# Kernel tuning notes

Hardware: AMD Instinct MI355X
Metric: run time of the kernel (lower is better)

The kernel has to match this reference:

```python
import jax, jax.numpy as jnp
import numpy as np

EPS = 1e-12  # matches torch F.normalize default eps

def l2norm(t):
    n = jnp.linalg.norm(t, axis=-1, keepdims=True)
    return t / jnp.maximum(n, EPS)

def rotate_half(x):
    # '... (j d) -> ... j d' with j=2: split into two halves, return cat(-x2, x1)
    x1, x2 = jnp.split(x, 2, axis=-1)
    return jnp.concatenate((-x2, x1), axis=-1)

def rotary_freqs(seq_len, dim):
    inv_freq = 1.0 / (10000.0 ** (jnp.arange(0, dim, 2, dtype=jnp.float32) / dim))
    seq = jnp.arange(seq_len, dtype=jnp.float32)
    freqs = seq[:, None] * inv_freq[None, :]          # [n, d/2]
    emb = jnp.concatenate((freqs, freqs), axis=-1)    # [n, d]
    return emb[None, None]                            # [1, 1, n, d]

def apply_rotary_pos_emb(t, freqs):
    # rot_dim == dim_head here, so the pass-through slice is empty
    return t * jnp.cos(freqs) + rotate_half(t) * jnp.sin(freqs)

def setup_inputs() -> dict:
    key = jax.random.key(0)
    kq, kk, kv = jax.random.split(key, 3)
    b, h, n, d = 2, 16, 2048, 64
    q = jax.random.normal(kq, (b, h, n, d), dtype=jnp.float32)
    k = jax.random.normal(kk, (b, h, n, d), dtype=jnp.float32)
    v = jax.random.normal(kv, (b, h, n, d), dtype=jnp.float32)
    q_scale = jnp.ones((d,), dtype=jnp.float32)
    k_scale = jnp.ones((d,), dtype=jnp.float32)
    return {"q": q, "k": k, "v": v, "q_scale": q_scale, "k_scale": k_scale}

def reference(q, k, v, q_scale, k_scale):
    b, h, n, d = q.shape
    # QK RMSNorm (l2 normalize + learned per-dim scale)
    q = l2norm(q) * q_scale
    k = l2norm(k) * k_scale
    # rotary position embedding (always applied in the source module)
    freqs = rotary_freqs(n, d)
    q = apply_rotary_pos_emb(q, freqs)
    k = apply_rotary_pos_emb(k, freqs)
    # attention: explicit scores -> softmax -> values
    scale = d ** -0.5
    sim = jnp.einsum('bhid,bhjd->bhij', q, k) * scale
    attn = jax.nn.softmax(sim, axis=-1)
    out = jnp.einsum('bhij,bhjd->bhid', attn, v)
    # 'b h n d -> b n (h d)'
    return out.transpose(0, 2, 1, 3).reshape(b, n, h * d)
```

## Files before the change

kernel.cpp:

```cpp
#include <hip/hip_runtime.h>
#include <math.h>

#define BH   32
#define NSEQ 2048
#define DH   64
#define NH   16
#define LOG2E 1.44269504088896f

typedef _Float16 f16x8 __attribute__((ext_vector_type(8)));
typedef __fp16   fp16x2 __attribute__((ext_vector_type(2)));
typedef _Float16 half2v __attribute__((ext_vector_type(2)));
typedef float    f32x16v __attribute__((ext_vector_type(16)));
typedef unsigned uint2v __attribute__((ext_vector_type(2)));

#if __has_builtin(__builtin_amdgcn_exp2f)
#define EXP2F(x) __builtin_amdgcn_exp2f(x)
#else
#define EXP2F(x) exp2f(x)
#endif

static __device__ __forceinline__ unsigned pkrtz(float a, float b) {
    fp16x2 r = __builtin_amdgcn_cvt_pkrtz(a, b);
    return __builtin_bit_cast(unsigned, r);
}
static __device__ __forceinline__ unsigned packh_rne(float a, float b) {
    union { _Float16 h[2]; unsigned u; } x;
    x.h[0] = (_Float16)a; x.h[1] = (_Float16)b;
    return x.u;
}

static __device__ __forceinline__ float2 rope_cs(int pos, int p) {
    float invf_rev = EXP2F(-(float)p * (13.287712379549449f / 32.0f)) * 0.15915494309189535f;
    float rev = (float)pos * invf_rev;
    float fr = rev - floorf(rev);
    float th = fr * 6.283185307179586f;
    return make_float2(__cosf(th), __sinf(th));
}

__global__ __launch_bounds__(256) void rope_tab_kernel(float4* __restrict__ tab) {
    const int id = blockIdx.x * 256 + threadIdx.x;
    const int pos = id >> 4, j = id & 15;
    float2 a = rope_cs(pos, 2 * j);
    float2 b = rope_cs(pos, 2 * j + 1);
    tab[id] = make_float4(a.x, a.y, b.x, b.y);
}

__global__ __launch_bounds__(256) void prep_all(
    const float* __restrict__ q, const float* __restrict__ k, const float* __restrict__ v,
    const float* __restrict__ qs, const float* __restrict__ ksc,
    const float4* __restrict__ tab,
    unsigned* __restrict__ qh, unsigned* __restrict__ kh, unsigned* __restrict__ vt2) {
    const int bid = blockIdx.x;
    const int t = threadIdx.x;
    if (bid < 4096) {
        const bool isq = bid < 2048;
        const float* in = isq ? q : k;
        const float* sc = isq ? qs : ksc;
        const float smul = isq ? 0.125f * LOG2E : 1.0f;
        const int sb = bid & 2047;
        const int r = t >> 3, l = t & 7;
        const int row = sb * 32 + r;
        const int pos = row & (NSEQ - 1);
        const float4* tb = tab + (pos << 4) + 4 * l;
        const float4 c0 = tb[0], c1 = tb[1], c2 = tb[2], c3 = tb[3];
        const float4 xa = *(const float4*)(in + (size_t)row * DH + 8 * l);
        const float4 xb = *(const float4*)(in + (size_t)row * DH + 8 * l + 4);
        float ss = xa.x * xa.x + xa.y * xa.y + xa.z * xa.z + xa.w * xa.w
                 + xb.x * xb.x + xb.y * xb.y + xb.z * xb.z + xb.w * xb.w;
        ss += __shfl_xor(ss, 1);
        ss += __shfl_xor(ss, 2);
        ss += __shfl_xor(ss, 4);
        const float inv = 1.0f / fmaxf(sqrtf(ss), 1e-12f);
        const float4 sa = *(const float4*)(sc + 8 * l);
        const float4 sb4 = *(const float4*)(sc + 8 * l + 4);
        float tv[8];
        tv[0] = xa.x * inv * sa.x;  tv[1] = xa.y * inv * sa.y;
        tv[2] = xa.z * inv * sa.z;  tv[3] = xa.w * inv * sa.w;
        tv[4] = xb.x * inv * sb4.x; tv[5] = xb.y * inv * sb4.y;
        tv[6] = xb.z * inv * sb4.z; tv[7] = xb.w * inv * sb4.w;
        float rv[8];
        #pragma unroll
        for (int e = 0; e < 8; ++e) {
            float p = __shfl_xor(tv[e], 4);
            rv[e] = (l < 4) ? -p : p;
        }
        float ov[8];
        ov[0] = (tv[0] * c0.x + rv[0] * c0.y) * smul;
        ov[1] = (tv[1] * c0.z + rv[1] * c0.w) * smul;
        ov[2] = (tv[2] * c1.x + rv[2] * c1.y) * smul;
        ov[3] = (tv[3] * c1.z + rv[3] * c1.w) * smul;
        ov[4] = (tv[4] * c2.x + rv[4] * c2.y) * smul;
        ov[5] = (tv[5] * c2.z + rv[5] * c2.w) * smul;
        ov[6] = (tv[6] * c3.x + rv[6] * c3.y) * smul;
        ov[7] = (tv[7] * c3.z + rv[7] * c3.w) * smul;
        const uint4 u4 = make_uint4(packh_rne(ov[0], ov[1]), packh_rne(ov[2], ov[3]),
                                    packh_rne(ov[4], ov[5]), packh_rne(ov[6], ov[7]));
        if (isq) {
            *(uint4*)(qh + row * 32 + 4 * l) = u4;
        } else {
            const int rloc = row & (NSEQ - 1);
            const unsigned idx = (unsigned)((rloc >> 5) * 1024 + (l >> 1) * 256
                               + (l & 1) * 128 + (rloc & 31) * 4);
            *(uint4*)(kh + (size_t)(row >> 11) * 65536 + idx) = u4;
        }
    } else {
        const int sb = bid - 4096;
        const int kt = sb & 31, bh = sb >> 5;
        __shared__ float Lv[64 * 68];
        #pragma unroll
        for (int i = 0; i < 4; ++i) {
            int chunk = t + 256 * i;
            int rr = chunk >> 4, fg = chunk & 15;
            *(float4*)&Lv[rr * 68 + fg * 4] =
                *(const float4*)(v + ((size_t)bh * NSEQ + kt * 64 + rr) * DH + fg * 4);
        }
        __syncthreads();
        const int d = t & 63, kg = t >> 6;
        unsigned u[8];
        #pragma unroll
        for (int j = 0; j < 8; ++j) {
            int ky = kg * 16 + 2 * j;
            u[j] = pkrtz(Lv[ky * 68 + d], Lv[(ky + 1) * 68 + d]);
        }
        const int rh = d >> 5, cc = d & 31;
        unsigned* dst = vt2 + (size_t)bh * 65536
                      + (size_t)((kt * 4 + kg) * 2 + rh) * 256 + cc * 4;
        *(uint4*)(dst)       = make_uint4(u[0], u[1], u[2], u[3]);
        *(uint4*)(dst + 128) = make_uint4(u[4], u[5], u[6], u[7]);
    }
}

static __device__ __forceinline__ f16x8 ld8(const unsigned* p) {
    return *(const f16x8*)p;
}

static __device__ __forceinline__ void load_k(f16x8 (&kd)[4], const unsigned* p) {
    #pragma unroll
    for (int ks = 0; ks < 4; ++ks) kd[ks] = ld8(p + ks * 256);
}
static __device__ __forceinline__ void load_v(f16x8 (&vd)[4], const unsigned* p) {
    #pragma unroll
    for (int kk = 0; kk < 2; ++kk)
        #pragma unroll
        for (int rh = 0; rh < 2; ++rh)
            vd[kk * 2 + rh] = ld8(p + kk * 512 + rh * 256);
}

static __device__ __forceinline__ void qk2(
    const f16x8 (&kc)[4], const f16x8 (&qf)[2][4], const f32x16v& z16,
    f32x16v& s0, f32x16v& s1)
{
    __builtin_amdgcn_s_setprio(1);
    s0 = __builtin_amdgcn_mfma_f32_32x32x16_f16(kc[0], qf[0][0], z16, 0, 0, 0);
    s1 = __builtin_amdgcn_mfma_f32_32x32x16_f16(kc[0], qf[1][0], z16, 0, 0, 0);
    #pragma unroll
    for (int ks = 1; ks < 4; ++ks) {
        s0 = __builtin_amdgcn_mfma_f32_32x32x16_f16(kc[ks], qf[0][ks], s0, 0, 0, 0);
        s1 = __builtin_amdgcn_mfma_f32_32x32x16_f16(kc[ks], qf[1][ks], s1, 0, 0, 0);
    }
    __builtin_amdgcn_s_setprio(0);
}

static __device__ __forceinline__ void pv_tile(
    f32x16v& s, const f16x8 (&vc)[4], f32x16v (&ot)[2], float& lp, int hf)
{
    #pragma unroll
    for (int r = 0; r < 16; ++r) s[r] = EXP2F(s[r]);
    #pragma unroll
    for (int kk = 0; kk < 2; ++kk) {
        unsigned P01 = pkrtz(s[kk * 8 + 0], s[kk * 8 + 1]);
        unsigned P23 = pkrtz(s[kk * 8 + 2], s[kk * 8 + 3]);
        unsigned P45 = pkrtz(s[kk * 8 + 4], s[kk * 8 + 5]);
        unsigned P67 = pkrtz(s[kk * 8 + 6], s[kk * 8 + 7]);
#if __has_builtin(__builtin_amdgcn_fdot2)
        const half2v one2 = {(_Float16)1.0f, (_Float16)1.0f};
        lp = __builtin_amdgcn_fdot2(__builtin_bit_cast(half2v, P01), one2, lp, false);
        lp = __builtin_amdgcn_fdot2(__builtin_bit_cast(half2v, P23), one2, lp, false);
        lp = __builtin_amdgcn_fdot2(__builtin_bit_cast(half2v, P45), one2, lp, false);
        lp = __builtin_amdgcn_fdot2(__builtin_bit_cast(half2v, P67), one2, lp, false);
#else
        #pragma unroll
        for (int r = 0; r < 8; ++r) lp += s[kk * 8 + r];
#endif
        union { unsigned u[4]; f16x8 v; } B;
#if __has_builtin(__builtin_amdgcn_permlane32_swap)
        uint2v r02 = __builtin_amdgcn_permlane32_swap(P01, P45, 0, 0);
        uint2v r13 = __builtin_amdgcn_permlane32_swap(P23, P67, 0, 0);
        B.u[0] = r02[0]; B.u[1] = r13[0]; B.u[2] = r02[1]; B.u[3] = r13[1];
#else
        unsigned x01 = (unsigned)__shfl_xor((int)P01, 32);
        unsigned x23 = (unsigned)__shfl_xor((int)P23, 32);
        unsigned x45 = (unsigned)__shfl_xor((int)P45, 32);
        unsigned x67 = (unsigned)__shfl_xor((int)P67, 32);
        B.u[0] = hf ? x45 : P01;
        B.u[1] = hf ? x67 : P23;
        B.u[2] = hf ? P45 : x01;
        B.u[3] = hf ? P67 : x23;
#endif
        __builtin_amdgcn_s_setprio(1);
        ot[0] = __builtin_amdgcn_mfma_f32_32x32x16_f16(vc[kk * 2 + 0], B.v, ot[0], 0, 0, 0);
        ot[1] = __builtin_amdgcn_mfma_f32_32x32x16_f16(vc[kk * 2 + 1], B.v, ot[1], 0, 0, 0);
        __builtin_amdgcn_s_setprio(0);
    }
}

static __device__ __forceinline__ void smpv2(
    f32x16v& s0, f32x16v& s1, const f16x8 (&vc)[4],
    f32x16v (&o)[2][2], float (&lp)[2], int hf)
{
    pv_tile(s0, vc, o[0], lp[0], hf);
    pv_tile(s1, vc, o[1], lp[1], hf);
}

__global__ __launch_bounds__(256, 2) void attn_kernel(
    const unsigned* __restrict__ qh, const unsigned* __restrict__ kf,
    const unsigned* __restrict__ vf, float* __restrict__ out) {

    __shared__ float Lred[128 * 33];

    const int flat = (blockIdx.x & 7) * 64 + (blockIdx.x >> 3);
    const int bh = flat >> 4, qb = flat & 15;

    const int tid = threadIdx.x;
    const int w = tid >> 6, lane = tid & 63;
    const int c = lane & 31, hf = lane >> 5;
    const int qhw = w & 1;
    const int khw = w >> 1;

    const _Float16* qbase = (const _Float16*)qh + ((size_t)bh * NSEQ + qb * 128) * DH;
    f16x8 qf[2][4];
    #pragma unroll
    for (int t = 0; t < 2; ++t)
        #pragma unroll
        for (int ks = 0; ks < 4; ++ks)
            qf[t][ks] = *(const f16x8*)(qbase + (t * 64 + qhw * 32 + c) * DH + ks * 16 + hf * 8);

    const unsigned* kfb = kf + (size_t)bh * 65536 + khw * 1024 + lane * 4;
    const unsigned* vfb = vf + (size_t)bh * 65536 + khw * 1024 + lane * 4;

    f32x16v z16;
    #pragma unroll
    for (int r = 0; r < 16; ++r) z16[r] = 0.f;

    f32x16v o[2][2];
    #pragma unroll
    for (int t = 0; t < 2; ++t)
        #pragma unroll
        for (int mt = 0; mt < 2; ++mt)
            #pragma unroll
            for (int r = 0; r < 16; ++r) o[t][mt][r] = 0.f;
    float lp[2] = {0.f, 0.f};

    f16x8 kc[4], vc[4];
    f32x16v sA0, sA1, sB0, sB1;

    load_k(kc, kfb);
    load_v(vc, vfb);
    qk2(kc, qf, z16, sA0, sA1);
    load_k(kc, kfb + 2048);

    for (int jt = 0; jt < 32; jt += 2) {
        qk2(kc, qf, z16, sB0, sB1);
        if (jt + 2 < 32) load_k(kc, kfb + (size_t)(jt + 2) * 2048);
        smpv2(sA0, sA1, vc, o, lp, hf);
        load_v(vc, vfb + (size_t)(jt + 1) * 2048);

        if (jt + 2 < 32) {
            qk2(kc, qf, z16, sA0, sA1);
            if (jt + 3 < 32) load_k(kc, kfb + (size_t)(jt + 3) * 2048);
        }
        smpv2(sB0, sB1, vc, o, lp, hf);
        if (jt + 2 < 32) load_v(vc, vfb + (size_t)(jt + 2) * 2048);
    }

    float lw[2];
    #pragma unroll
    for (int t = 0; t < 2; ++t) lw[t] = lp[t] + __shfl_xor(lp[t], 32);

    const int b = bh >> 4, h = bh & 15;
    #pragma unroll
    for (int t = 0; t < 2; ++t) {
        if (t) __syncthreads();
        if (w >= 2) {
            const int base = ((w - 2) * 64 + lane) * 33;
            f32x16v* ov = (t == 0) ? &o[0][0] : &o[1][0];
            #pragma unroll
            for (int mt = 0; mt < 2; ++mt)
                #pragma unroll
                for (int r = 0; r < 16; ++r) Lred[base + mt * 16 + r] = ov[mt][r];
            Lred[base + 32] = lw[t];
        }
        __syncthreads();
        if (w < 2) {
            const int base = (w * 64 + lane) * 33;
            f32x16v* ov = (t == 0) ? &o[0][0] : &o[1][0];
            #pragma unroll
            for (int mt = 0; mt < 2; ++mt)
                #pragma unroll
                for (int r = 0; r < 16; ++r) ov[mt][r] += Lred[base + mt * 16 + r];
            float invl = 1.0f / (lw[t] + Lred[base + 32]);
            const int pos = qb * 128 + t * 64 + w * 32 + c;
            float* obase = out + ((size_t)b * NSEQ + pos) * (NH * DH) + h * DH;
            #pragma unroll
            for (int mt = 0; mt < 2; ++mt)
                #pragma unroll
                for (int g = 0; g < 4; ++g) {
                    float4 r4 = make_float4(ov[mt][g * 4 + 0] * invl, ov[mt][g * 4 + 1] * invl,
                                            ov[mt][g * 4 + 2] * invl, ov[mt][g * 4 + 3] * invl);
                    *(float4*)(obase + mt * 32 + g * 8 + hf * 4) = r4;
                }
        }
    }
}

extern "C" void kernel_launch(void* const* d_in, const int* in_sizes, int n_in,
                              void* d_out, int out_size, void* d_ws, size_t ws_size,
                              hipStream_t stream) {
    const float* q  = (const float*)d_in[0];
    const float* k  = (const float*)d_in[1];
    const float* v  = (const float*)d_in[2];
    const float* qs = (const float*)d_in[3];
    const float* ks = (const float*)d_in[4];
    float* outp = (float*)d_out;

    unsigned* qh  = (unsigned*)d_ws;
    unsigned* kh  = qh + (size_t)BH * NSEQ * 32;
    unsigned* vt2 = kh + (size_t)BH * NSEQ * 32;
    float4*   tab = (float4*)(vt2 + (size_t)BH * NSEQ * 32);

    rope_tab_kernel<<<128, 256, 0, stream>>>(tab);
    prep_all<<<5120, 256, 0, stream>>>(q, k, v, qs, ks, tab, qh, kh, vt2);
    attn_kernel<<<512, 256, 0, stream>>>(qh, kh, vt2, outp);
}
```

Before: 139.1 us.

## Split attention key range across two blocks and merge partials in a separate kernel

Each query block is now processed by two workgroups, each covering half of the key sequence, which doubles the grid to 1024 blocks and raises the occupancy hint to 3. Unnormalized partial outputs and row sums go to the output buffer and a workspace buffer, and a new merge kernel adds them and normalizes. The intent is more parallelism and better latency hiding on a GPU with many CUs. The cost is extra global traffic for the partial writes and reads plus one more kernel launch. If the workspace is too small, the original single kernel is used instead.

After: 146.4 us. 5.3% more time.

```diff
diff --git a/kernel.cpp b/kernel.cpp
--- a/kernel.cpp
+++ b/kernel.cpp
@@ -6,6 +6,7 @@
 #define DH   64
 #define NH   16
 #define LOG2E 1.44269504088896f
+#define NJTS 16
 
 typedef _Float16 f16x8 __attribute__((ext_vector_type(8)));
 typedef __fp16   fp16x2 __attribute__((ext_vector_type(2)));
@@ -133,7 +134,6 @@
 static __device__ __forceinline__ f16x8 ld8(const unsigned* p) {
     return *(const f16x8*)p;
 }
-
 static __device__ __forceinline__ void load_k(f16x8 (&kd)[4], const unsigned* p) {
     #pragma unroll
     for (int ks = 0; ks < 4; ++ks) kd[ks] = ld8(p + ks * 256);
@@ -144,6 +144,18 @@
         #pragma unroll
         for (int rh = 0; rh < 2; ++rh)
             vd[kk * 2 + rh] = ld8(p + kk * 512 + rh * 256);
+}
+
+static __device__ __forceinline__ f32x16v qk1(
+    const f16x8 (&kc)[4], const f16x8 (&q)[4], const f32x16v& z16)
+{
+    __builtin_amdgcn_s_setprio(1);
+    f32x16v s = __builtin_amdgcn_mfma_f32_32x32x16_f16(kc[0], q[0], z16, 0, 0, 0);
+    #pragma unroll
+    for (int ks = 1; ks < 4; ++ks)
+        s = __builtin_amdgcn_mfma_f32_32x32x16_f16(kc[ks], q[ks], s, 0, 0, 0);
+    __builtin_amdgcn_s_setprio(0);
+    return s;
 }
 
 static __device__ __forceinline__ void qk2(
@@ -212,13 +224,18 @@
     pv_tile(s1, vc, o[1], lp[1], hf);
 }
 
-__global__ __launch_bounds__(256, 2) void attn_kernel(
+__global__ __launch_bounds__(256, 3) void attn_split(
     const unsigned* __restrict__ qh, const unsigned* __restrict__ kf,
-    const unsigned* __restrict__ vf, float* __restrict__ out) {
+    const unsigned* __restrict__ vf, float* __restrict__ o0buf,
+    float* __restrict__ o1buf, float* __restrict__ l0buf,
+    float* __restrict__ l1buf) {
 
     __shared__ float Lred[128 * 33];
 
-    const int flat = (blockIdx.x & 7) * 64 + (blockIdx.x >> 3);
+    const int bid = blockIdx.x;
+    const int h = bid & 1;
+    const int rest = bid >> 1;
+    const int flat = (rest & 7) * 64 + (rest >> 3);
     const int bh = flat >> 4, qb = flat & 15;
 
     const int tid = threadIdx.x;
@@ -235,6 +252,100 @@
         for (int ks = 0; ks < 4; ++ks)
             qf[t][ks] = *(const f16x8*)(qbase + (t * 64 + qhw * 32 + c) * DH + ks * 16 + hf * 8);
 
+    const unsigned* kfp = kf + (size_t)bh * 65536 + (size_t)h * NJTS * 2048 + khw * 1024 + lane * 4;
+    const unsigned* vfp = vf + (size_t)bh * 65536 + (size_t)h * NJTS * 2048 + khw * 1024 + lane * 4;
+
+    f32x16v z16;
+    #pragma unroll
+    for (int r = 0; r < 16; ++r) z16[r] = 0.f;
+
+    f32x16v o[2][2];
+    #pragma unroll
+    for (int t = 0; t < 2; ++t)
+        #pragma unroll
+        for (int mt = 0; mt < 2; ++mt)
+            #pragma unroll
+            for (int r = 0; r < 16; ++r) o[t][mt][r] = 0.f;
+    float lp[2] = {0.f, 0.f};
+
+    f16x8 kc[4], vc[4];
+    load_k(kc, kfp);
+    load_v(vc, vfp);
+
+    for (int jt = 0; jt < NJTS; ++jt) {
+        f32x16v s = qk1(kc, qf[0], z16);
+        pv_tile(s, vc, o[0], lp[0], hf);
+        s = qk1(kc, qf[1], z16);
+        if (jt + 1 < NJTS) load_k(kc, kfp + (size_t)(jt + 1) * 2048);
+        pv_tile(s, vc, o[1], lp[1], hf);
+        if (jt + 1 < NJTS) load_v(vc, vfp + (size_t)(jt + 1) * 2048);
+    }
+
+    float lw[2];
+    #pragma unroll
+    for (int t = 0; t < 2; ++t) lw[t] = lp[t] + __shfl_xor(lp[t], 32);
+
+    const int b = bh >> 4, hh = bh & 15;
+    #pragma unroll
+    for (int t = 0; t < 2; ++t) {
+        if (t) __syncthreads();
+        if (w >= 2) {
+            const int base = ((w - 2) * 64 + lane) * 33;
+            f32x16v* ov = (t == 0) ? &o[0][0] : &o[1][0];
+            #pragma unroll
+            for (int mt = 0; mt < 2; ++mt)
+                #pragma unroll
+                for (int r = 0; r < 16; ++r) Lred[base + mt * 16 + r] = ov[mt][r];
+            Lred[base + 32] = lw[t];
+        }
+        __syncthreads();
+        if (w < 2) {
+            const int base = (w * 64 + lane) * 33;
+            f32x16v* ov = (t == 0) ? &o[0][0] : &o[1][0];
+            #pragma unroll
+            for (int mt = 0; mt < 2; ++mt)
+                #pragma unroll
+                for (int r = 0; r < 16; ++r) ov[mt][r] += Lred[base + mt * 16 + r];
+            const float ltot = lw[t] + Lred[base + 32];
+            const int pos = qb * 128 + t * 64 + w * 32 + c;
+            float* obase = (h ? o1buf : o0buf)
+                         + ((size_t)b * NSEQ + pos) * (NH * DH) + hh * DH;
+            #pragma unroll
+            for (int mt = 0; mt < 2; ++mt)
+                #pragma unroll
+                for (int g = 0; g < 4; ++g) {
+                    float4 r4 = make_float4(ov[mt][g * 4 + 0], ov[mt][g * 4 + 1],
+                                            ov[mt][g * 4 + 2], ov[mt][g * 4 + 3]);
+                    *(float4*)(obase + mt * 32 + g * 8 + hf * 4) = r4;
+                }
+            if (hf == 0) (h ? l1buf : l0buf)[(size_t)bh * NSEQ + pos] = ltot;
+        }
+    }
+}
+
+__global__ __launch_bounds__(256, 2) void attn_kernel(
+    const unsigned* __restrict__ qh, const unsigned* __restrict__ kf,
+    const unsigned* __restrict__ vf, float* __restrict__ out) {
+
+    __shared__ float Lred[128 * 33];
+
+    const int flat = (blockIdx.x & 7) * 64 + (blockIdx.x >> 3);
+    const int bh = flat >> 4, qb = flat & 15;
+
+    const int tid = threadIdx.x;
+    const int w = tid >> 6, lane = tid & 63;
+    const int c = lane & 31, hf = lane >> 5;
+    const int qhw = w & 1;
+    const int khw = w >> 1;
+
+    const _Float16* qbase = (const _Float16*)qh + ((size_t)bh * NSEQ + qb * 128) * DH;
+    f16x8 qf[2][4];
+    #pragma unroll
+    for (int t = 0; t < 2; ++t)
+        #pragma unroll
+        for (int ks = 0; ks < 4; ++ks)
+            qf[t][ks] = *(const f16x8*)(qbase + (t * 64 + qhw * 32 + c) * DH + ks * 16 + hf * 8);
+
     const unsigned* kfb = kf + (size_t)bh * 65536 + khw * 1024 + lane * 4;
     const unsigned* vfb = vf + (size_t)bh * 65536 + khw * 1024 + lane * 4;
 
@@ -310,6 +421,26 @@
                     *(float4*)(obase + mt * 32 + g * 8 + hf * 4) = r4;
                 }
         }
+    }
+}
+
+__global__ __launch_bounds__(256) void merge_kernel(
+    float* __restrict__ out, const float* __restrict__ o1,
+    const float* __restrict__ l0, const float* __restrict__ l1) {
+    const int t = blockIdx.x * 256 + threadIdx.x;
+    #pragma unroll
+    for (int i = 0; i < 2; ++i) {
+        const int f = t + i * 524288;
+        const int fi = f * 4;
+        const int b  = fi >> 21;
+        const int n  = (fi >> 10) & 2047;
+        const int hh = (fi >> 6) & 15;
+        const int li = ((b << 4) + hh) * NSEQ + n;
+        const float inv = 1.0f / (l0[li] + l1[li]);
+        float4 a = *(const float4*)(out + fi);
+        float4 c = *(const float4*)(o1 + fi);
+        *(float4*)(out + fi) = make_float4((a.x + c.x) * inv, (a.y + c.y) * inv,
+                                           (a.z + c.z) * inv, (a.w + c.w) * inv);
     }
 }
 
@@ -327,8 +458,17 @@
     unsigned* kh  = qh + (size_t)BH * NSEQ * 32;
     unsigned* vt2 = kh + (size_t)BH * NSEQ * 32;
     float4*   tab = (float4*)(vt2 + (size_t)BH * NSEQ * 32);
+    float*    pO1 = (float*)(tab + 32768);
+    float*    l0  = pO1 + (size_t)2 * NSEQ * NH * DH;
+    float*    l1  = l0 + (size_t)BH * NSEQ;
+    const size_t NEED = (size_t)((char*)(l1 + (size_t)BH * NSEQ) - (char*)d_ws);
 
     rope_tab_kernel<<<128, 256, 0, stream>>>(tab);
     prep_all<<<5120, 256, 0, stream>>>(q, k, v, qs, ks, tab, qh, kh, vt2);
-    attn_kernel<<<512, 256, 0, stream>>>(qh, kh, vt2, outp);
-}
+    if (ws_size >= NEED) {
+        attn_split<<<1024, 256, 0, stream>>>(qh, kh, vt2, outp, pO1, l0, l1);
+        merge_kernel<<<2048, 256, 0, stream>>>(outp, pO1, l0, l1);
+    } else {
+        attn_kernel<<<512, 256, 0, stream>>>(qh, kh, vt2, outp);
+    }
+}
```

## Fuse Q normalization and rotary embedding into attention kernel prologue

Applied to the files above, without the earlier changes.

Moves the Q l2-norm, scale, rotary rotation and fp16 packing out of the prep kernel and into the attention kernel's Q-fragment load, so prep only handles K and V. This removes the fp16 Q write to workspace and its read back, and shrinks the prep grid. In exchange each attention block reads fp32 Q (twice the bytes) and does the norm and rope math in the prologue, which adds registers and latency before the main loop. Several waves in a block may also redo the same Q rows.

Result: no change. 140.2 us (+0.8%).

```diff
diff --git a/kernel.cpp b/kernel.cpp
--- a/kernel.cpp
+++ b/kernel.cpp
@@ -46,33 +46,28 @@
 }
 
 __global__ __launch_bounds__(256) void prep_all(
-    const float* __restrict__ q, const float* __restrict__ k, const float* __restrict__ v,
-    const float* __restrict__ qs, const float* __restrict__ ksc,
-    const float4* __restrict__ tab,
-    unsigned* __restrict__ qh, unsigned* __restrict__ kh, unsigned* __restrict__ vt2) {
+    const float* __restrict__ k, const float* __restrict__ v,
+    const float* __restrict__ ksc, const float4* __restrict__ tab,
+    unsigned* __restrict__ kh, unsigned* __restrict__ vt2) {
     const int bid = blockIdx.x;
     const int t = threadIdx.x;
-    if (bid < 4096) {
-        const bool isq = bid < 2048;
-        const float* in = isq ? q : k;
-        const float* sc = isq ? qs : ksc;
-        const float smul = isq ? 0.125f * LOG2E : 1.0f;
-        const int sb = bid & 2047;
+    if (bid < 2048) {
+        const int sb = bid;
         const int r = t >> 3, l = t & 7;
         const int row = sb * 32 + r;
         const int pos = row & (NSEQ - 1);
         const float4* tb = tab + (pos << 4) + 4 * l;
         const float4 c0 = tb[0], c1 = tb[1], c2 = tb[2], c3 = tb[3];
-        const float4 xa = *(const float4*)(in + (size_t)row * DH + 8 * l);
-        const float4 xb = *(const float4*)(in + (size_t)row * DH + 8 * l + 4);
+        const float4 xa = *(const float4*)(k + (size_t)row * DH + 8 * l);
+        const float4 xb = *(const float4*)(k + (size_t)row * DH + 8 * l + 4);
         float ss = xa.x * xa.x + xa.y * xa.y + xa.z * xa.z + xa.w * xa.w
                  + xb.x * xb.x + xb.y * xb.y + xb.z * xb.z + xb.w * xb.w;
         ss += __shfl_xor(ss, 1);
         ss += __shfl_xor(ss, 2);
         ss += __shfl_xor(ss, 4);
         const float inv = 1.0f / fmaxf(sqrtf(ss), 1e-12f);
-        const float4 sa = *(const float4*)(sc + 8 * l);
-        const float4 sb4 = *(const float4*)(sc + 8 * l + 4);
+        const float4 sa = *(const float4*)(ksc + 8 * l);
+        const float4 sb4 = *(const float4*)(ksc + 8 * l + 4);
         float tv[8];
         tv[0] = xa.x * inv * sa.x;  tv[1] = xa.y * inv * sa.y;
         tv[2] = xa.z * inv * sa.z;  tv[3] = xa.w * inv * sa.w;
@@ -85,26 +80,22 @@
             rv[e] = (l < 4) ? -p : p;
         }
         float ov[8];
-        ov[0] = (tv[0] * c0.x + rv[0] * c0.y) * smul;
-        ov[1] = (tv[1] * c0.z + rv[1] * c0.w) * smul;
-        ov[2] = (tv[2] * c1.x + rv[2] * c1.y) * smul;
-        ov[3] = (tv[3] * c1.z + rv[3] * c1.w) * smul;
-        ov[4] = (tv[4] * c2.x + rv[4] * c2.y) * smul;
-        ov[5] = (tv[5] * c2.z + rv[5] * c2.w) * smul;
-        ov[6] = (tv[6] * c3.x + rv[6] * c3.y) * smul;
-        ov[7] = (tv[7] * c3.z + rv[7] * c3.w) * smul;
+        ov[0] = tv[0] * c0.x + rv[0] * c0.y;
+        ov[1] = tv[1] * c0.z + rv[1] * c0.w;
+        ov[2] = tv[2] * c1.x + rv[2] * c1.y;
+        ov[3] = tv[3] * c1.z + rv[3] * c1.w;
+        ov[4] = tv[4] * c2.x + rv[4] * c2.y;
+        ov[5] = tv[5] * c2.z + rv[5] * c2.w;
+        ov[6] = tv[6] * c3.x + rv[6] * c3.y;
+        ov[7] = tv[7] * c3.z + rv[7] * c3.w;
         const uint4 u4 = make_uint4(packh_rne(ov[0], ov[1]), packh_rne(ov[2], ov[3]),
                                     packh_rne(ov[4], ov[5]), packh_rne(ov[6], ov[7]));
-        if (isq) {
-            *(uint4*)(qh + row * 32 + 4 * l) = u4;
-        } else {
-            const int rloc = row & (NSEQ - 1);
-            const unsigned idx = (unsigned)((rloc >> 5) * 1024 + (l >> 1) * 256
-                               + (l & 1) * 128 + (rloc & 31) * 4);
-            *(uint4*)(kh + (size_t)(row >> 11) * 65536 + idx) = u4;
-        }
+        const int rloc = row & (NSEQ - 1);
+        const unsigned idx = (unsigned)((rloc >> 5) * 1024 + (l >> 1) * 256
+                           + (l & 1) * 128 + (rloc & 31) * 4);
+        *(uint4*)(kh + (size_t)(row >> 11) * 65536 + idx) = u4;
     } else {
-        const int sb = bid - 4096;
+        const int sb = bid - 2048;
         const int kt = sb & 31, bh = sb >> 5;
         __shared__ float Lv[64 * 68];
         #pragma unroll
@@ -213,7 +204,8 @@
 }
 
 __global__ __launch_bounds__(256, 2) void attn_kernel(
-    const unsigned* __restrict__ qh, const unsigned* __restrict__ kf,
+    const float* __restrict__ q, const float* __restrict__ qsc,
+    const float4* __restrict__ tab, const unsigned* __restrict__ kf,
     const unsigned* __restrict__ vf, float* __restrict__ out) {
 
     __shared__ float Lred[128 * 33];
@@ -227,13 +219,51 @@
     const int qhw = w & 1;
     const int khw = w >> 1;
 
-    const _Float16* qbase = (const _Float16*)qh + ((size_t)bh * NSEQ + qb * 128) * DH;
+    const float smulq = 0.125f * LOG2E;
     f16x8 qf[2][4];
     #pragma unroll
-    for (int t = 0; t < 2; ++t)
-        #pragma unroll
-        for (int ks = 0; ks < 4; ++ks)
-            qf[t][ks] = *(const f16x8*)(qbase + (t * 64 + qhw * 32 + c) * DH + ks * 16 + hf * 8);
+    for (int t = 0; t < 2; ++t) {
+        const int n = qb * 128 + t * 64 + qhw * 32 + c;
+        const float* qrow = q + ((size_t)bh * NSEQ + n) * DH;
+        float tv[4][8];
+        float own = 0.f;
+        #pragma unroll
+        for (int ks = 0; ks < 4; ++ks) {
+            const float4 a  = *(const float4*)(qrow + ks * 16 + hf * 8);
+            const float4 b4 = *(const float4*)(qrow + ks * 16 + hf * 8 + 4);
+            tv[ks][0] = a.x;  tv[ks][1] = a.y;  tv[ks][2] = a.z;  tv[ks][3] = a.w;
+            tv[ks][4] = b4.x; tv[ks][5] = b4.y; tv[ks][6] = b4.z; tv[ks][7] = b4.w;
+            own += a.x * a.x + a.y * a.y + a.z * a.z + a.w * a.w
+                 + b4.x * b4.x + b4.y * b4.y + b4.z * b4.z + b4.w * b4.w;
+        }
+        const float ss = own + __shfl_xor(own, 32);
+        const float inv = 1.0f / fmaxf(sqrtf(ss), 1e-12f);
+        #pragma unroll
+        for (int ks = 0; ks < 4; ++ks) {
+            const float4 sa  = *(const float4*)(qsc + ks * 16 + hf * 8);
+            const float4 sb4 = *(const float4*)(qsc + ks * 16 + hf * 8 + 4);
+            tv[ks][0] *= inv * sa.x;  tv[ks][1] *= inv * sa.y;
+            tv[ks][2] *= inv * sa.z;  tv[ks][3] *= inv * sa.w;
+            tv[ks][4] *= inv * sb4.x; tv[ks][5] *= inv * sb4.y;
+            tv[ks][6] *= inv * sb4.z; tv[ks][7] *= inv * sb4.w;
+        }
+        #pragma unroll
+        for (int ks = 0; ks < 4; ++ks) {
+            const int jb = ((ks & 1) * 16 + hf * 8) >> 1;
+            const float sgn = (ks < 2) ? -1.f : 1.f;
+            union { unsigned u[4]; f16x8 v; } U;
+            #pragma unroll
+            for (int e2 = 0; e2 < 4; ++e2) {
+                const float4 ct = tab[(n << 4) + jb + e2];
+                const float r0 = sgn * tv[ks ^ 2][2 * e2];
+                const float r1 = sgn * tv[ks ^ 2][2 * e2 + 1];
+                const float o0 = (tv[ks][2 * e2]     * ct.x + r0 * ct.y) * smulq;
+                const float o1 = (tv[ks][2 * e2 + 1] * ct.z + r1 * ct.w) * smulq;
+                U.u[e2] = packh_rne(o0, o1);
+            }
+            qf[t][ks] = U.v;
+        }
+    }
 
     const unsigned* kfb = kf + (size_t)bh * 65536 + khw * 1024 + lane * 4;
     const unsigned* vfb = vf + (size_t)bh * 65536 + khw * 1024 + lane * 4;
@@ -323,12 +353,11 @@
     const float* ks = (const float*)d_in[4];
     float* outp = (float*)d_out;
 
-    unsigned* qh  = (unsigned*)d_ws;
-    unsigned* kh  = qh + (size_t)BH * NSEQ * 32;
+    unsigned* kh  = (unsigned*)d_ws;
     unsigned* vt2 = kh + (size_t)BH * NSEQ * 32;
     float4*   tab = (float4*)(vt2 + (size_t)BH * NSEQ * 32);
 
     rope_tab_kernel<<<128, 256, 0, stream>>>(tab);
-    prep_all<<<5120, 256, 0, stream>>>(q, k, v, qs, ks, tab, qh, kh, vt2);
-    attn_kernel<<<512, 256, 0, stream>>>(qh, kh, vt2, outp);
-}
+    prep_all<<<3072, 256, 0, stream>>>(k, v, ks, tab, kh, vt2);
+    attn_kernel<<<512, 256, 0, stream>>>(q, qs, tab, kh, vt2, outp);
+}
```
